# Kernel optimization log

Measured on AMD Instinct MI355X. Metric: run time of the kernel, lower is better.

The kernel has to match this reference:

```python
import jax, jax.numpy as jnp
import numpy as np

B, T, C, H = 4, 2048, 1024, 16

def setup_inputs() -> dict:
    key = jax.random.key(0)
    k1, k2, k3, k4, k5 = jax.random.split(key, 5)
    s = 1.0 / np.sqrt(C)
    return {
        "x": jax.random.normal(k1, (B, T, C), dtype=jnp.float32),
        "w_attn": jax.random.normal(k2, (C, 3 * C), dtype=jnp.float32) * s,
        "b_attn": jax.random.normal(k3, (3 * C,), dtype=jnp.float32) * 0.02,
        "w_proj": jax.random.normal(k4, (C, C), dtype=jnp.float32) * s,
        "b_proj": jax.random.normal(k5, (C,), dtype=jnp.float32) * 0.02,
    }

def reference(x, w_attn, b_attn, w_proj, b_proj):
    Bx, Tx, Cx = x.shape
    hd = Cx // H  # head_size
    qkv = x @ w_attn + b_attn                      # [B,T,3C]
    q, k, v = jnp.split(qkv, 3, axis=2)
    # [B,T,C] -> [B,H,T,hd]
    def heads(t):
        return t.reshape(Bx, Tx, H, hd).transpose(0, 2, 1, 3)
    q, k, v = heads(q), heads(k), heads(v)
    scale = hd ** -0.5
    scores = jnp.einsum("bhqd,bhkd->bhqk", q, k) * scale  # [B,H,T,T]
    causal = jnp.tril(jnp.ones((Tx, Tx), dtype=bool))
    scores = jnp.where(causal[None, None], scores, -jnp.inf)
    probs = jax.nn.softmax(scores, axis=-1)
    attn = jnp.einsum("bhqk,bhkd->bhqd", probs, v)  # [B,H,T,hd]
    attn = attn.transpose(0, 2, 1, 3).reshape(Bx, Tx, Cx)
    return attn @ w_proj + b_proj
```

## Files before the change

kernel.cpp:

```cpp
#include <hip/hip_runtime.h>
#include <hip/hip_bf16.h>

#define BATCH 4
#define TSEQ  2048
#define CDIM  1024
#define NHEAD 16
#define HDIM  64
#define C3    3072
#define MROWS (BATCH * TSEQ)

#define QSCALE 0.18033688011112f

typedef short bf16x8 __attribute__((ext_vector_type(8)));
typedef short short8 __attribute__((ext_vector_type(8)));
typedef __bf16 bf16v8 __attribute__((ext_vector_type(8)));
typedef float f32x4 __attribute__((ext_vector_type(4)));

#define AS1 __attribute__((address_space(1)))
#define AS3 __attribute__((address_space(3)))

#if __has_builtin(__builtin_amdgcn_exp2f)
#define EXP2F(x) __builtin_amdgcn_exp2f(x)
#else
#define EXP2F(x) exp2f(x)
#endif

__device__ __forceinline__ short f2bf(float x) {
    unsigned int u = __builtin_bit_cast(unsigned int, x);
    u += 0x7fffu + ((u >> 16) & 1u);
    return (short)(u >> 16);
}

__device__ __forceinline__ unsigned int cvtpk(float lo, float hi) {
    unsigned int r;
    asm("v_cvt_pk_bf16_f32 %0, %1, %2" : "=v"(r) : "v"(lo), "v"(hi));
    return r;
}

__device__ __forceinline__ f32x4 mfma16(bf16x8 a, bf16x8 b, f32x4 c) {
    return __builtin_amdgcn_mfma_f32_16x16x32_bf16(
        __builtin_bit_cast(bf16v8, a), __builtin_bit_cast(bf16v8, b), c, 0, 0, 0);
}

__global__ void prep_kernel(const float* __restrict__ x, short* __restrict__ x_bf,
                            const float* __restrict__ wA, short* __restrict__ wAT,
                            const float* __restrict__ wP, short* __restrict__ wPT,
                            float qs) {
    const int tx = threadIdx.x, ty = threadIdx.y;
    if (blockIdx.z == 0) {
        const int i = (blockIdx.y * 128 + blockIdx.x) * 256 + ty * 32 + tx;
        float4 a = ((const float4*)x)[2 * i];
        float4 b = ((const float4*)x)[2 * i + 1];
        short8 o;
        o[0] = f2bf(a.x); o[1] = f2bf(a.y); o[2] = f2bf(a.z); o[3] = f2bf(a.w);
        o[4] = f2bf(b.x); o[5] = f2bf(b.y); o[6] = f2bf(b.z); o[7] = f2bf(b.w);
        ((short8*)x_bf)[i] = o;
        return;
    }
    const float* in;
    short* out;
    int N, qcols;
    float sc;
    if (blockIdx.z == 1) {
        if (blockIdx.x >= C3 / 32) return;
        in = wA; out = wAT; N = C3; qcols = CDIM; sc = qs;
    } else {
        if (blockIdx.x >= CDIM / 32) return;
        in = wP; out = wPT; N = CDIM; qcols = 0; sc = 1.0f;
    }
    __shared__ float tile[32][33];
    const int n0 = blockIdx.x * 32, k0 = blockIdx.y * 32;
#pragma unroll
    for (int j = 0; j < 4; ++j)
        tile[ty + j * 8][tx] = in[(size_t)(k0 + ty + j * 8) * N + n0 + tx];
    __syncthreads();
#pragma unroll
    for (int j = 0; j < 4; ++j) {
        const int n = n0 + ty + j * 8;
        const float s = (n < qcols) ? sc : 1.0f;
        out[(size_t)n * CDIM + k0 + tx] = f2bf(tile[tx][ty + j * 8] * s);
    }
}

template <typename OutT, int WAVES_M, int WAVES_N, int BN>
__global__ __launch_bounds__(512, 4) void gemm3_kernel(
    const short* __restrict__ A, const short* __restrict__ Bt,
    const float* __restrict__ bias, OutT* __restrict__ out,
    int M, int N, int K, int qcols, float qs) {
    constexpr int BM = 128;
    constexpr int MF = BM / (WAVES_M * 16);
    constexpr int NF = BN / (WAVES_N * 16);
    constexpr int BLOADS = BN / 128;
    __shared__ alignas(16) short Ab[3][BM * 32];
    __shared__ alignas(16) short Bb[3][BN * 32];

    const int tid = threadIdx.x;
    const int lane = tid & 63;
    const int w = tid >> 6;
    const int wm = w / WAVES_N;
    const int wn = w % WAVES_N;

    const int nwg = gridDim.x * gridDim.y;
    const int lid = blockIdx.y * gridDim.x + blockIdx.x;
    const int swz = (lid & 7) * (nwg >> 3) + (lid >> 3);
    const int m0 = (swz / gridDim.x) * BM;
    const int n0 = (swz % gridDim.x) * BN;

    const int NT = K >> 5;

    const int fr = lane & 15;
    const int ch = lane >> 4;

    f32x4 acc[MF][NF] = {};

    const int rA  = tid >> 2;
    const int lcA = (tid & 3) ^ ((rA >> 1) & 3);
    const short* gA = A + (size_t)(m0 + rA) * K + lcA * 8;
    const short* gB[BLOADS];
#pragma unroll
    for (int i = 0; i < BLOADS; ++i) {
        const int s = tid + i * 512;
        const int r = s >> 2;
        const int lc = (s & 3) ^ ((r >> 1) & 3);
        gB[i] = Bt + (size_t)(n0 + r) * K + lc * 8;
    }

    int aoff[MF], boff[NF];
#pragma unroll
    for (int f = 0; f < MF; ++f) {
        const int r = wm * (BM / WAVES_M) + f * 16 + fr;
        aoff[f] = r * 32 + (ch ^ ((r >> 1) & 3)) * 8;
    }
#pragma unroll
    for (int f = 0; f < NF; ++f) {
        const int r = wn * (BN / WAVES_N) + f * 16 + fr;
        boff[f] = r * 32 + (ch ^ ((r >> 1) & 3)) * 8;
    }

#define GSTAGE(buf, kt)                                                          \
    do {                                                                         \
        __builtin_amdgcn_global_load_lds((const AS1 void*)(gA + (kt)),           \
            (AS3 void*)&Ab[buf][w * 512], 16, 0, 0);                             \
        _Pragma("unroll")                                                        \
        for (int i = 0; i < BLOADS; ++i)                                         \
            __builtin_amdgcn_global_load_lds((const AS1 void*)(gB[i] + (kt)),    \
                (AS3 void*)&Bb[buf][i * 4096 + w * 512], 16, 0, 0);              \
    } while (0)

#define GITER(BUF, T)                                                            \
    do {                                                                         \
        if constexpr (BLOADS == 2) {                                             \
            asm volatile("s_waitcnt vmcnt(3)" ::: "memory");                     \
        } else {                                                                 \
            asm volatile("s_waitcnt vmcnt(2)" ::: "memory");                     \
        }                                                                        \
        __builtin_amdgcn_s_barrier();                                            \
        const int ktn = (((T) + 2 < NT) ? ((T) + 2) : 0) * 32;                   \
        GSTAGE((BUF + 2) % 3, ktn);                                              \
        __builtin_amdgcn_sched_barrier(0);                                       \
        bf16x8 af[MF], bfv[NF];                                                  \
        _Pragma("unroll")                                                        \
        for (int f = 0; f < MF; ++f)                                             \
            af[f] = *(const bf16x8*)&Ab[BUF][aoff[f]];                           \
        _Pragma("unroll")                                                        \
        for (int f = 0; f < NF; ++f)                                             \
            bfv[f] = *(const bf16x8*)&Bb[BUF][boff[f]];                          \
        _Pragma("unroll")                                                        \
        for (int mf = 0; mf < MF; ++mf)                                          \
            _Pragma("unroll")                                                    \
            for (int nf = 0; nf < NF; ++nf)                                      \
                acc[mf][nf] = mfma16(af[mf], bfv[nf], acc[mf][nf]);              \
    } while (0)

    GSTAGE(0, 0);
    GSTAGE(1, 32);

    int t = 0;
    for (; t + 3 <= NT; t += 3) {
        GITER(0, t);
        GITER(1, t + 1);
        GITER(2, t + 2);
    }
    if (t < NT) { GITER(0, t); ++t; }
    if (t < NT) { GITER(1, t); }
#undef GITER
#undef GSTAGE

    const int r0 = (lane >> 4) * 4;
    const int cn = lane & 15;
#pragma unroll
    for (int mf = 0; mf < MF; ++mf) {
#pragma unroll
        for (int nf = 0; nf < NF; ++nf) {
            const int col = n0 + wn * (BN / WAVES_N) + nf * 16 + cn;
            const float bv = bias[col] * ((col < qcols) ? qs : 1.0f);
#pragma unroll
            for (int r = 0; r < 4; ++r) {
                const int row = m0 + wm * (BM / WAVES_M) + mf * 16 + r0 + r;
                const float v = acc[mf][nf][r] + bv;
                if constexpr (sizeof(OutT) == 2)
                    out[(size_t)row * N + col] = (OutT)f2bf(v);
                else
                    out[(size_t)row * N + col] = (OutT)v;
            }
        }
    }
}

template <int BUF>
__device__ __forceinline__ void attn_iter(
    int KB, int niter, int qrow, int w, int cn, int g, int kg8,
    int krow, int kx0, int kx1, int skv, int sd0,
    const short* kgl, size_t ksrc, const short* vbase,
    short (*klds)[64 * 64], short (*vt)[64 * 72],
    const bf16x8 (&qf)[2][2], f32x4 (&ao)[2][4], f32x4 (&ao4)[2],
    const bf16x8& vones) {

    const int kvb = KB * 64;
    const bool pf = (KB + 1 < niter);

    bf16x8 r0, r1;
    if (pf) {
        r0 = *(const bf16x8*)(vbase + (size_t)(kvb + 64 + skv) * C3 + sd0);
        r1 = *(const bf16x8*)(vbase + (size_t)(kvb + 64 + skv + 1) * C3 + sd0);
        const short* kn = kgl + ksrc + (size_t)(kvb + 64) * C3;
        __builtin_amdgcn_global_load_lds((const AS1 void*)kn,
            (AS3 void*)&klds[BUF ^ 1][w * 512], 16, 0, 0);
        __builtin_amdgcn_global_load_lds((const AS1 void*)(kn + (size_t)32 * C3),
            (AS3 void*)&klds[BUF ^ 1][2048 + w * 512], 16, 0, 0);
    }

    if (kvb <= qrow + 31) {
        bf16x8 kf[4][2];
#pragma unroll
        for (int t = 0; t < 4; ++t) {
            const int rb = t * 1024 + krow;
            kf[t][0] = *(const bf16x8*)&klds[BUF][rb + kx0];
            kf[t][1] = *(const bf16x8*)&klds[BUF][rb + kx1];
        }

        bf16x8 vf[2][4];
#pragma unroll
        for (int c = 0; c < 2; ++c)
#pragma unroll
            for (int dt = 0; dt < 4; ++dt)
                vf[c][dt] = *(const bf16x8*)&vt[BUF][(dt * 16 + cn) * 72 + c * 32 + kg8];

#pragma unroll
        for (int qt = 0; qt < 2; ++qt) {
            const int qrow16 = qrow + qt * 16;

            f32x4 s[4] = {};
#pragma unroll
            for (int t = 0; t < 4; ++t) {
                s[t] = mfma16(kf[t][0], qf[qt][0], s[t]);
                s[t] = mfma16(kf[t][1], qf[qt][1], s[t]);
            }

            const bool maskIter = (kvb + 63 > qrow16);
            float p[4][4];
            if (maskIter) {
#pragma unroll
                for (int t = 0; t < 4; ++t)
#pragma unroll
                    for (int r = 0; r < 4; ++r) {
                        const int kv = kvb + t * 16 + 4 * g + r;
                        const int q  = qrow16 + cn;
                        float e = EXP2F(s[t][r]);
                        p[t][r] = (kv > q) ? 0.f : e;
                    }
            } else {
#pragma unroll
                for (int t = 0; t < 4; ++t)
#pragma unroll
                    for (int r = 0; r < 4; ++r)
                        p[t][r] = EXP2F(s[t][r]);
            }

            unsigned int wq[8];
#pragma unroll
            for (int t = 0; t < 4; ++t) {
                wq[t * 2 + 0] = cvtpk(p[t][0], p[t][1]);
                wq[t * 2 + 1] = cvtpk(p[t][2], p[t][3]);
            }

#pragma unroll
            for (int c = 0; c < 2; ++c) {
                union { unsigned int u[4]; bf16x8 v; } pu;
                unsigned int p0 = wq[4 * c + 0], p2 = wq[4 * c + 2];
                asm("v_permlane32_swap_b32 %0, %1" : "+v"(p0), "+v"(p2));
                asm("v_permlane16_swap_b32 %0, %1" : "+v"(p0), "+v"(p2));
                pu.u[0] = p0; pu.u[2] = p2;
                unsigned int p1 = wq[4 * c + 1], p3 = wq[4 * c + 3];
                asm("v_permlane32_swap_b32 %0, %1" : "+v"(p1), "+v"(p3));
                asm("v_permlane16_swap_b32 %0, %1" : "+v"(p1), "+v"(p3));
                pu.u[1] = p1; pu.u[3] = p3;
#pragma unroll
                for (int dt = 0; dt < 4; ++dt)
                    ao[qt][dt] = mfma16(pu.v, vf[c][dt], ao[qt][dt]);
                ao4[qt] = mfma16(pu.v, vones, ao4[qt]);
            }
        }
    }

    if (pf) {
#pragma unroll
        for (int i = 0; i < 8; ++i) {
            unsigned int pk = (unsigned short)r0[i] | ((unsigned int)(unsigned short)r1[i] << 16);
            *(unsigned int*)&vt[BUF ^ 1][(sd0 + i) * 72 + skv] = pk;
        }
    }
    __syncthreads();
}

__global__ __launch_bounds__(256) void attn_kernel(const short* __restrict__ qkv,
                                                   short* __restrict__ attn_out) {
    __shared__ short vt[2][64 * 72];
    __shared__ short klds[2][64 * 64];

    const int tid = threadIdx.x;
    const int lane = tid & 63;
    const int w = tid >> 6;

    const int bid = blockIdx.x;
    const int swz = (bid & 7) * 64 + (bid >> 3);
    const int bh = swz >> 3;
    const int pairp = swz & 7;
    const int b = bh >> 4;
    const int h = bh & 15;

    const size_t base = (size_t)b * TSEQ * C3 + (size_t)h * HDIM;
    const int cn = lane & 15;
    const int g = lane >> 4;
    const int kg8 = g * 8;

    const bf16x8 vones = {0x3F80, 0x3F80, 0x3F80, 0x3F80,
                          0x3F80, 0x3F80, 0x3F80, 0x3F80};

    const short* kgl = qkv + base + 1024;
    const size_t ksrc = (size_t)(w * 8 + (lane >> 3)) * C3 + ((lane & 7) ^ (lane >> 3)) * 8;
    const int cnl = cn & 7;
    const int krow = cn * 64;
    const int kx0 = ((g ^ cnl) * 8);
    const int kx1 = (((g ^ 4) ^ cnl) * 8);

    const int skv = (tid & 31) * 2;
    const int sd0 = (tid >> 5) * 8;
    const short* vbase = qkv + base + 2048;

    for (int pass = 0; pass < 2; ++pass) {
        const int qi = pass ? pairp : (15 - pairp);
        const int q0 = qi * 128;
        const int qrow = q0 + w * 32;
        const int niter = 2 * qi + 2;

        bf16x8 qf[2][2];
#pragma unroll
        for (int qt = 0; qt < 2; ++qt)
#pragma unroll
            for (int ks = 0; ks < 2; ++ks)
                qf[qt][ks] = *(const bf16x8*)(qkv + base +
                    (size_t)(qrow + qt * 16 + cn) * C3 + ks * 32 + kg8);

        f32x4 ao[2][4] = {};
        f32x4 ao4[2] = {};

        {
            __builtin_amdgcn_global_load_lds((const AS1 void*)(kgl + ksrc),
                                             (AS3 void*)&klds[0][w * 512], 16, 0, 0);
            __builtin_amdgcn_global_load_lds((const AS1 void*)(kgl + ksrc + (size_t)32 * C3),
                                             (AS3 void*)&klds[0][2048 + w * 512], 16, 0, 0);
            bf16x8 r0 = *(const bf16x8*)(vbase + (size_t)skv * C3 + sd0);
            bf16x8 r1 = *(const bf16x8*)(vbase + (size_t)(skv + 1) * C3 + sd0);
#pragma unroll
            for (int i = 0; i < 8; ++i) {
                unsigned int pk = (unsigned short)r0[i] | ((unsigned int)(unsigned short)r1[i] << 16);
                *(unsigned int*)&vt[0][(sd0 + i) * 72 + skv] = pk;
            }
        }
        __syncthreads();

        int kb = 0;
        for (; kb + 2 <= niter; kb += 2) {
            attn_iter<0>(kb,     niter, qrow, w, cn, g, kg8, krow, kx0, kx1,
                         skv, sd0, kgl, ksrc, vbase, klds, vt, qf, ao, ao4, vones);
            attn_iter<1>(kb + 1, niter, qrow, w, cn, g, kg8, krow, kx0, kx1,
                         skv, sd0, kgl, ksrc, vbase, klds, vt, qf, ao, ao4, vones);
        }

#pragma unroll
        for (int qt = 0; qt < 2; ++qt) {
#pragma unroll
            for (int r = 0; r < 4; ++r) {
                const float lr = 1.0f / ao4[qt][r];
                const int q = qrow + qt * 16 + 4 * g + r;
#pragma unroll
                for (int dt = 0; dt < 4; ++dt)
                    attn_out[(size_t)(b * TSEQ + q) * CDIM + h * HDIM + dt * 16 + cn] =
                        f2bf(ao[qt][dt][r] * lr);
            }
        }
        __syncthreads();
    }
}

extern "C" void kernel_launch(void* const* d_in, const int* in_sizes, int n_in,
                              void* d_out, int out_size, void* d_ws, size_t ws_size,
                              hipStream_t stream) {
    const float* x      = (const float*)d_in[0];
    const float* w_attn = (const float*)d_in[1];
    const float* b_attn = (const float*)d_in[2];
    const float* w_proj = (const float*)d_in[3];
    const float* b_proj = (const float*)d_in[4];
    float* out = (float*)d_out;

    char* ws = (char*)d_ws;
    short* x_bf   = (short*)ws;
    short* wqkvT  = (short*)(ws + (16u << 20));
    short* wprojT = (short*)(ws + (22u << 20));
    short* qkv    = (short*)(ws + (24u << 20));

    prep_kernel<<<dim3(128, 32, 3), dim3(32, 8), 0, stream>>>(
        x, x_bf, w_attn, wqkvT, w_proj, wprojT, QSCALE);

    gemm3_kernel<short, 2, 4, 256><<<dim3(C3 / 256, MROWS / 128), 512, 0, stream>>>(
        x_bf, wqkvT, b_attn, qkv, MROWS, C3, CDIM, CDIM, QSCALE);

    attn_kernel<<<dim3(512), 256, 0, stream>>>(qkv, x_bf);

    gemm3_kernel<float, 4, 2, 128><<<dim3(CDIM / 128, MROWS / 128), 512, 0, stream>>>(
        x_bf, wprojT, b_proj, out, MROWS, CDIM, CDIM, 0, 1.0f);
}
```

Measured before the change: 158.0 us.

## Triple-buffer K tiles in LDS and relax per-iteration barrier waits

Moves the K-tile async global-to-LDS loads from a double-buffered to a triple-buffered ring, so each K tile is prefetched two iterations ahead. The per-iteration __syncthreads is replaced by an explicit LDS-only waitcnt plus s_barrier, which lets the async K loads stay in flight across the barrier. The main loop is unrolled by three with a remainder tail. The cost is one more 8 KB K buffer in LDS, which may lower occupancy. Correctness also rests on the implicit vmcnt ordering of global_load_lds, which is fragile.

```diff
diff --git a/kernel.cpp b/kernel.cpp
--- a/kernel.cpp
+++ b/kernel.cpp
@@ -218,16 +218,18 @@
 
     const int kvb = KB * 64;
     const bool pf = (KB + 1 < niter);
+    const int vcur = KB & 1;
 
     bf16x8 r0, r1;
     if (pf) {
         r0 = *(const bf16x8*)(vbase + (size_t)(kvb + 64 + skv) * C3 + sd0);
         r1 = *(const bf16x8*)(vbase + (size_t)(kvb + 64 + skv + 1) * C3 + sd0);
-        const short* kn = kgl + ksrc + (size_t)(kvb + 64) * C3;
+        const int kt2 = (KB + 2 < niter) ? (kvb + 128) : 0;
+        const short* kn = kgl + ksrc + (size_t)kt2 * C3;
         __builtin_amdgcn_global_load_lds((const AS1 void*)kn,
-            (AS3 void*)&klds[BUF ^ 1][w * 512], 16, 0, 0);
+            (AS3 void*)&klds[(BUF + 2) % 3][w * 512], 16, 0, 0);
         __builtin_amdgcn_global_load_lds((const AS1 void*)(kn + (size_t)32 * C3),
-            (AS3 void*)&klds[BUF ^ 1][2048 + w * 512], 16, 0, 0);
+            (AS3 void*)&klds[(BUF + 2) % 3][2048 + w * 512], 16, 0, 0);
     }
 
     if (kvb <= qrow + 31) {
@@ -244,7 +246,7 @@
         for (int c = 0; c < 2; ++c)
 #pragma unroll
             for (int dt = 0; dt < 4; ++dt)
-                vf[c][dt] = *(const bf16x8*)&vt[BUF][(dt * 16 + cn) * 72 + c * 32 + kg8];
+                vf[c][dt] = *(const bf16x8*)&vt[vcur][(dt * 16 + cn) * 72 + c * 32 + kg8];
 
 #pragma unroll
         for (int qt = 0; qt < 2; ++qt) {
@@ -307,16 +309,17 @@
 #pragma unroll
         for (int i = 0; i < 8; ++i) {
             unsigned int pk = (unsigned short)r0[i] | ((unsigned int)(unsigned short)r1[i] << 16);
-            *(unsigned int*)&vt[BUF ^ 1][(sd0 + i) * 72 + skv] = pk;
-        }
-    }
-    __syncthreads();
+            *(unsigned int*)&vt[vcur ^ 1][(sd0 + i) * 72 + skv] = pk;
+        }
+    }
+    asm volatile("s_waitcnt lgkmcnt(0)" ::: "memory");
+    __builtin_amdgcn_s_barrier();
 }
 
 __global__ __launch_bounds__(256) void attn_kernel(const short* __restrict__ qkv,
                                                    short* __restrict__ attn_out) {
     __shared__ short vt[2][64 * 72];
-    __shared__ short klds[2][64 * 64];
+    __shared__ short klds[3][64 * 64];
 
     const int tid = threadIdx.x;
     const int lane = tid & 63;
@@ -366,25 +369,41 @@
         f32x4 ao4[2] = {};
 
         {
+            bf16x8 r0 = *(const bf16x8*)(vbase + (size_t)skv * C3 + sd0);
+            bf16x8 r1 = *(const bf16x8*)(vbase + (size_t)(skv + 1) * C3 + sd0);
             __builtin_amdgcn_global_load_lds((const AS1 void*)(kgl + ksrc),
                                              (AS3 void*)&klds[0][w * 512], 16, 0, 0);
             __builtin_amdgcn_global_load_lds((const AS1 void*)(kgl + ksrc + (size_t)32 * C3),
                                              (AS3 void*)&klds[0][2048 + w * 512], 16, 0, 0);
-            bf16x8 r0 = *(const bf16x8*)(vbase + (size_t)skv * C3 + sd0);
-            bf16x8 r1 = *(const bf16x8*)(vbase + (size_t)(skv + 1) * C3 + sd0);
+            __builtin_amdgcn_global_load_lds((const AS1 void*)(kgl + ksrc + (size_t)64 * C3),
+                                             (AS3 void*)&klds[1][w * 512], 16, 0, 0);
+            __builtin_amdgcn_global_load_lds((const AS1 void*)(kgl + ksrc + (size_t)96 * C3),
+                                             (AS3 void*)&klds[1][2048 + w * 512], 16, 0, 0);
 #pragma unroll
             for (int i = 0; i < 8; ++i) {
                 unsigned int pk = (unsigned short)r0[i] | ((unsigned int)(unsigned short)r1[i] << 16);
                 *(unsigned int*)&vt[0][(sd0 + i) * 72 + skv] = pk;
             }
-        }
-        __syncthreads();
+            asm volatile("s_waitcnt vmcnt(2) lgkmcnt(0)" ::: "memory");
+            __builtin_amdgcn_s_barrier();
+        }
 
         int kb = 0;
-        for (; kb + 2 <= niter; kb += 2) {
+        for (; kb + 3 <= niter; kb += 3) {
             attn_iter<0>(kb,     niter, qrow, w, cn, g, kg8, krow, kx0, kx1,
                          skv, sd0, kgl, ksrc, vbase, klds, vt, qf, ao, ao4, vones);
             attn_iter<1>(kb + 1, niter, qrow, w, cn, g, kg8, krow, kx0, kx1,
+                         skv, sd0, kgl, ksrc, vbase, klds, vt, qf, ao, ao4, vones);
+            attn_iter<2>(kb + 2, niter, qrow, w, cn, g, kg8, krow, kx0, kx1,
+                         skv, sd0, kgl, ksrc, vbase, klds, vt, qf, ao, ao4, vones);
+        }
+        if (kb < niter) {
+            attn_iter<0>(kb, niter, qrow, w, cn, g, kg8, krow, kx0, kx1,
+                         skv, sd0, kgl, ksrc, vbase, klds, vt, qf, ao, ao4, vones);
+            ++kb;
+        }
+        if (kb < niter) {
+            attn_iter<1>(kb, niter, qrow, w, cn, g, kg8, krow, kx0, kx1,
                          skv, sd0, kgl, ksrc, vbase, klds, vt, qf, ao, ao4, vones);
         }
 
```

Result: no change. 161.0 us (+1.9%).
